# Optimization experiments

Hardware: AMD Instinct MI355X
Metric: run time of the kernel (lower is better)

The kernel has to match this reference:

```python
import jax, jax.numpy as jnp
import numpy as np

NSAMPLE = 32
EPS = 1e-5


def _fps(xyz, npoint):
    # xyz: [B, N, 3] -> indices [B, npoint] (farthest point sampling, start at idx 0)
    B, N, _ = xyz.shape
    def body(i, state):
        idx, dist, far = state
        idx = idx.at[:, i].set(far)
        centroid = jnp.take_along_axis(xyz, far[:, None, None], axis=1)  # [B,1,3]
        d = jnp.sum((xyz - centroid) ** 2, axis=-1)                      # [B,N]
        dist = jnp.minimum(dist, d)
        far = jnp.argmax(dist, axis=-1).astype(jnp.int32)
        return idx, dist, far
    idx0 = jnp.zeros((B, npoint), jnp.int32)
    dist0 = jnp.full((B, N), 1e10, xyz.dtype)
    far0 = jnp.zeros((B,), jnp.int32)
    idx, _, _ = jax.lax.fori_loop(0, npoint, body, (idx0, dist0, far0))
    return idx


def _knn(query, ref, k):
    # query [B,S,3], ref [B,N,3] -> neighbor idx [B,S,k]
    d = (jnp.sum(query * query, -1)[:, :, None]
         - 2.0 * jnp.einsum('bsc,bnc->bsn', query, ref)
         + jnp.sum(ref * ref, -1)[:, None, :])
    _, idx = jax.lax.top_k(-d, k)
    return idx


def _gather(x, idx):
    # x [B,N,C], idx [B,S,K] -> [B,S,K,C]
    B, S, K = idx.shape
    out = jnp.take_along_axis(x, idx.reshape(B, S * K)[..., None], axis=1)
    return out.reshape(B, S, K, x.shape[-1])


def _set_abstraction(xyz, feat, npoint, weights):
    # xyz [B,N,3], feat [B,N,C]
    fidx = _fps(xyz, npoint)
    new_xyz = jnp.take_along_axis(xyz, fidx[..., None], axis=1)        # [B,S,3]
    nidx = _knn(new_xyz, xyz, NSAMPLE)                                 # [B,S,K]
    g_xyz = _gather(xyz, nidx) - new_xyz[:, :, None, :]                # [B,S,K,3]
    g_feat = _gather(feat, nidx)                                       # [B,S,K,C]
    x = jnp.concatenate([g_xyz, g_feat], axis=-1)                      # [B,S,K,3+C]
    for W in weights:  # 1x1 conv == per-point matmul, then InstanceNorm2d (affine=False) + ReLU
        x = jnp.einsum('bskc,cd->bskd', x, W)
        mu = jnp.mean(x, axis=(1, 2), keepdims=True)
        var = jnp.var(x, axis=(1, 2), keepdims=True)
        x = jax.nn.relu((x - mu) * jax.lax.rsqrt(var + EPS))
    new_feat = jnp.max(x, axis=2)                                      # [B,S,Cout]
    return new_xyz, new_feat, fidx


def setup_inputs() -> dict:
    key = jax.random.key(0)
    ks = jax.random.split(key, 8)
    B, N = 4, 16384
    pc = jax.random.normal(ks[0], (B, 3, N), jnp.float32)
    feature = jax.random.normal(ks[1], (B, 3, N), jnp.float32)
    def w(k, cin, cout):
        return jax.random.normal(k, (cin, cout), jnp.float32) / np.sqrt(cin).astype(np.float32)
    return {
        'pc': pc, 'feature': feature,
        'sa1_w1': w(ks[2], 6, 32),  'sa1_w2': w(ks[3], 32, 32), 'sa1_w3': w(ks[4], 32, 32),
        'sa2_w1': w(ks[5], 35, 64), 'sa2_w2': w(ks[6], 64, 64), 'sa2_w3': w(ks[7], 64, 64),
    }


def reference(pc, feature, sa1_w1, sa1_w2, sa1_w3, sa2_w1, sa2_w2, sa2_w3):
    NPOINT = 4096
    xyz = jnp.transpose(pc, (0, 2, 1))       # [B,N,3]
    feat = jnp.transpose(feature, (0, 2, 1))  # [B,N,3]
    xyz1, feat1, fidx1 = _set_abstraction(xyz, feat, NPOINT // 2, [sa1_w1, sa1_w2, sa1_w3])
    xyz2, feat2, fidx2 = _set_abstraction(xyz1, feat1, NPOINT // 4, [sa2_w1, sa2_w2, sa2_w3])
    # match torch channel-first layout on outputs
    pc_l1 = jnp.transpose(xyz1, (0, 2, 1))
    pc_l2 = jnp.transpose(xyz2, (0, 2, 1))
    feat_l2 = jnp.transpose(feat2, (0, 2, 1))  # [B,64,NPOINT//4]
    return (pc, pc_l1, pc_l2, feat_l2, fidx1, fidx2)
```

## Files before the change

### kernel.cpp

```cpp
#include <hip/hip_runtime.h>
#include <math.h>

namespace {

constexpr int BB = 4;
constexpr int N0 = 16384;
constexpr int S1 = 2048;
constexpr int S2 = 1024;

__device__ __forceinline__ float sq3(float x, float y, float z){
  #pragma clang fp contract(off)
  return x*x + y*y + z*z;
}
__device__ __forceinline__ float sqdist(float ax,float ay,float az,float bx,float by,float bz){
  #pragma clang fp contract(off)
  float dx = ax-bx; float dy = ay-by; float dz = az-bz;
  return dx*dx + dy*dy + dz*dz;
}
__device__ __forceinline__ float dot3(float ax,float ay,float az,float bx,float by,float bz){
  #pragma clang fp contract(off)
  return ax*bx + ay*by + az*bz;
}
__device__ __forceinline__ float knndist(float qs, float dot, float rs){
  #pragma clang fp contract(off)
  return (qs - 2.0f*dot) + rs;
}

__global__ __launch_bounds__(256) void k_setup(const float* __restrict__ pc,
                                               const float* __restrict__ feat,
                                               float* __restrict__ out_pc,
                                               float* __restrict__ xyz,
                                               float* __restrict__ fN,
                                               float* __restrict__ rsq0)
{
  int t = blockIdx.x*256 + threadIdx.x;
  if (t < BB*3*N0) out_pc[t] = pc[t];
  if (t < BB*N0){
    int b = t >> 14, n = t & (N0-1);
    const float* p = pc + (size_t)b*3*N0;
    float x = p[n], y = p[N0+n], z = p[2*N0+n];
    float* q = xyz + (size_t)t*3;
    q[0]=x; q[1]=y; q[2]=z;
    rsq0[t] = sq3(x,y,z);
    const float* f = feat + (size_t)b*3*N0;
    float* g = fN + (size_t)t*3;
    g[0]=f[n]; g[1]=f[N0+n]; g[2]=f[2*N0+n];
  }
}

__device__ __forceinline__ void fps_writeout(int b, int i, float cx, float cy, float cz, int far,
                                             float* sxyz, float* srsq, float* pcl, float* fidxf, int NP)
{
  fidxf[(size_t)b*NP + i] = (float)far;
  float* o = sxyz + ((size_t)b*NP + i)*3;
  o[0]=cx; o[1]=cy; o[2]=cz;
  float* pb = pcl + (size_t)b*3*NP;
  pb[i] = cx; pb[NP+i] = cy; pb[2*NP+i] = cz;
  srsq[(size_t)b*NP + i] = sq3(cx,cy,cz);
}

template<int N, int NP, int BS, int PPT>
__global__ __launch_bounds__(BS) void k_fps(const float* __restrict__ pts,
                                            float* __restrict__ sxyz,
                                            float* __restrict__ srsq,
                                            float* __restrict__ pcl,
                                            float* __restrict__ fidxf)
{
  static_assert(N == BS*PPT, "bad fps shape");
  constexpr int NW = BS/64;
  int b = blockIdx.x, t = threadIdx.x;
  int lane = t & 63;
  int wid  = t >> 6;
  const float* P = pts + (size_t)b*N*3;
  float px[PPT], py[PPT], pz[PPT], dist[PPT];
  #pragma unroll
  for (int j=0;j<PPT;j++){
    int g = t + BS*j;
    px[j]=P[g*3]; py[j]=P[g*3+1]; pz[j]=P[g*3+2];
    dist[j]=1e10f;
  }
  __shared__ unsigned long long slot[2][NW];
  float cx = P[0], cy = P[1], cz = P[2];
  if (t == 0) fps_writeout(b, 0, cx, cy, cz, 0, sxyz, srsq, pcl, fidxf, NP);
  for (int i=1;i<NP;i++){
    int par = i & 1;
    float msq = -1.0f;
    #pragma unroll
    for (int j=0;j<PPT;j++){
      float d  = sqdist(px[j],py[j],pz[j],cx,cy,cz);
      float nd = fminf(dist[j], d);
      dist[j]  = nd;
      msq = fmaxf(msq, nd);
    }
    float s = sqrtf(msq);
    unsigned xb = __float_as_uint(msq);
    while (xb > 0u && sqrtf(__uint_as_float(xb - 1u)) == s) xb--;
    float lo = __uint_as_float(xb);
    int li = 0x7FFFFFFF;
    #pragma unroll
    for (int j=PPT-1;j>=0;j--) if (dist[j] >= lo) li = t + BS*j;
    unsigned long long key = ((unsigned long long)__float_as_uint(s) << 32)
                           | (unsigned long long)(unsigned)(~li);
    #pragma unroll
    for (int off=32; off>0; off>>=1){
      unsigned long long o = __shfl_xor(key, off);
      key = (o > key) ? o : key;
    }
    if (lane == 0) slot[par][wid] = key;
    __syncthreads();
    unsigned long long best = slot[par][0];
    #pragma unroll
    for (int w=1; w<NW; w++){
      unsigned long long o = slot[par][w];
      best = (o > best) ? o : best;
    }
    int far = (int)(~(unsigned)best);
    far = __builtin_amdgcn_readfirstlane(far);
    cx = P[(size_t)far*3]; cy = P[(size_t)far*3+1]; cz = P[(size_t)far*3+2];
    if (t == 0) fps_writeout(b, i, cx, cy, cz, far, sxyz, srsq, pcl, fidxf, NP);
  }
}

template<int NREF, int PPT, int NQ>
__global__ __launch_bounds__(512) void k_knn(const float* __restrict__ qxyz,
                                             const float* __restrict__ qrsq,
                                             const float* __restrict__ rxyz,
                                             const float* __restrict__ rrsq,
                                             int* __restrict__ nidx)
{
  static_assert(NREF == 512*PPT, "bad knn shape");
  int q = blockIdx.x;
  int b = q / NQ;
  int t = threadIdx.x;
  const float* R  = rxyz + (size_t)b*NREF*3;
  const float* RS = rrsq + (size_t)b*NREF;
  float qx = qxyz[(size_t)q*3], qy = qxyz[(size_t)q*3+1], qz = qxyz[(size_t)q*3+2];
  float qs = qrsq[q];
  unsigned u[PPT];
  #pragma unroll
  for (int j=0;j<PPT;j++){
    int g = t + 512*j;
    float rx=R[g*3], ry=R[g*3+1], rz=R[g*3+2];
    float d = knndist(qs, dot3(qx,qy,qz,rx,ry,rz), RS[g]);
    unsigned bu = __float_as_uint(d);
    u[j] = ((int)bu < 0) ? ~bu : (bu | 0x80000000u);
  }
  __shared__ unsigned hist[256];
  __shared__ unsigned s_pref, s_pm, s_want, s_cnteq;
  __shared__ int s_n;
  __shared__ int s_eq[1024];
  __shared__ int s_ne;
  if (t == 0){ s_pref=0u; s_pm=0u; s_want=32u; s_n=0; s_ne=0; }

  for (int shift=24; shift>=0; shift-=8){
    if (t < 256) hist[t] = 0u;
    __syncthreads();
    unsigned pref = s_pref, pm = s_pm;
    #pragma unroll
    for (int j=0;j<PPT;j++){
      if ((u[j] & pm) == pref) atomicAdd(&hist[(u[j]>>shift)&255], 1u);
    }
    __syncthreads();
    if (t < 64){
      unsigned h0=hist[4*t], h1=hist[4*t+1], h2=hist[4*t+2], h3=hist[4*t+3];
      unsigned ssum = h0+h1+h2+h3;
      unsigned inc = ssum;
      #pragma unroll
      for (int off=1; off<64; off<<=1){
        unsigned o = __shfl_up(inc, off);
        if (t >= off) inc += o;
      }
      unsigned exc = inc - ssum;
      unsigned want = s_want;
      if (exc < want && want <= inc){
        unsigned rem = want - exc;
        unsigned bin, below;
        if      (rem <= h0)       { bin=4*t+0; below=exc; }
        else if (rem <= h0+h1)    { bin=4*t+1; below=exc+h0; }
        else if (rem <= h0+h1+h2) { bin=4*t+2; below=exc+h0+h1; }
        else                      { bin=4*t+3; below=exc+h0+h1+h2; }
        s_pref = pref | (bin << shift);
        s_pm   = pm   | (0xFFu << shift);
        s_want = want - below;
        if (shift == 0) s_cnteq = hist[bin];
      }
    }
    __syncthreads();
  }
  unsigned T = s_pref;
  unsigned krem = s_want;
  unsigned cnteq = s_cnteq;
  int* outq = nidx + (size_t)q*32;
  #pragma unroll
  for (int j=0;j<PPT;j++){
    if (u[j] < T){ int p = atomicAdd(&s_n, 1); outq[p] = t + 512*j; }
  }
  __syncthreads();
  if (cnteq == krem){
    #pragma unroll
    for (int j=0;j<PPT;j++){
      if (u[j] == T){ int p = atomicAdd(&s_n, 1); outq[p] = t + 512*j; }
    }
  } else {
    #pragma unroll
    for (int j=0;j<PPT;j++){
      if (u[j] == T){ int p = atomicAdd(&s_ne, 1); if (p < 1024) s_eq[p] = t + 512*j; }
    }
    __syncthreads();
    if (t == 0){
      int ne = s_ne; if (ne > 1024) ne = 1024;
      int p = s_n;
      int take = (int)krem; if (take > ne) take = ne;
      for (int r=0; r<take; r++){
        int mn = 0x7FFFFFFF, mi = -1;
        for (int e=0; e<ne; e++){ if (s_eq[e] < mn){ mn = s_eq[e]; mi = e; } }
        if (mi < 0) break;
        outq[p++] = mn;
        s_eq[mi] = 0x7FFFFFFF;
      }
    }
  }
}

template<int C>
__device__ __forceinline__ void accum_sums(const float* o, int b, float* sums){
  __shared__ float s_sum[C];
  __shared__ float s_ssq[C];
  int t = threadIdx.x;
  if (t < C){ s_sum[t]=0.f; s_ssq[t]=0.f; }
  __syncthreads();
  int lane = t & 63;
  #pragma unroll
  for (int c=0;c<C;c++){
    float v = o[c], v2 = v*v;
    #pragma unroll
    for (int off=32; off>0; off>>=1){ v += __shfl_down(v, off); v2 += __shfl_down(v2, off); }
    if (lane == 0){ atomicAdd(&s_sum[c], v); atomicAdd(&s_ssq[c], v2); }
  }
  __syncthreads();
  if (t < C){
    atomicAdd(&sums[(b*64+t)*2],   s_sum[t]);
    atomicAdd(&sums[(b*64+t)*2+1], s_ssq[t]);
  }
}

__global__ __launch_bounds__(256) void k_sa1_l1(const float* __restrict__ xyz,
                                                const float* __restrict__ fN,
                                                const float* __restrict__ sxyz,
                                                const int* __restrict__ nidx,
                                                const float* __restrict__ W,
                                                float* __restrict__ xout,
                                                float* __restrict__ sums)
{
  __shared__ float sW[192];
  int t = threadIdx.x;
  if (t < 192) sW[t] = W[t];
  int row = blockIdx.x*256 + t;
  int b = row >> 16;
  int sk = row & 65535;
  int s = sk >> 5;
  int nb = nidx[row];
  const float* pr = xyz  + ((size_t)(b*N0 + nb))*3;
  const float* pq = sxyz + ((size_t)(b*S1 + s ))*3;
  const float* pf = fN   + ((size_t)(b*N0 + nb))*3;
  float i0 = pr[0]-pq[0], i1 = pr[1]-pq[1], i2 = pr[2]-pq[2];
  float i3 = pf[0], i4 = pf[1], i5 = pf[2];
  __syncthreads();
  float o[32];
  #pragma unroll
  for (int c=0;c<32;c++){
    float a = i0*sW[c];
    a = fmaf(i1, sW[ 32+c], a);
    a = fmaf(i2, sW[ 64+c], a);
    a = fmaf(i3, sW[ 96+c], a);
    a = fmaf(i4, sW[128+c], a);
    a = fmaf(i5, sW[160+c], a);
    o[c] = a;
    xout[(size_t)c*262144 + row] = a;
  }
  accum_sums<32>(o, b, sums);
}

template<int CIN, int COUT, int LRPB>
__global__ __launch_bounds__(256) void k_sa_mid(const float* __restrict__ xin,
                                                const float* __restrict__ W,
                                                const float* __restrict__ sums_in,
                                                float* __restrict__ xout,
                                                float* __restrict__ sums_out,
                                                int rows_total, float invM)
{
  __shared__ float sW[CIN*COUT];
  __shared__ float s_mu[CIN];
  __shared__ float s_rs[CIN];
  int t = threadIdx.x;
  int row = blockIdx.x*256 + t;
  int bb = (blockIdx.x*256) >> LRPB;
  for (int i=t; i<CIN*COUT; i+=256) sW[i] = W[i];
  if (t < CIN){
    float sm = sums_in[(bb*64+t)*2], sq = sums_in[(bb*64+t)*2+1];
    float mu = sm*invM;
    float var = fmaxf(sq*invM - mu*mu, 0.f);
    s_mu[t] = mu;
    s_rs[t] = 1.0f/sqrtf(var + 1e-5f);
  }
  __syncthreads();
  float o[COUT];
  #pragma unroll
  for (int d=0;d<COUT;d++) o[d] = 0.f;
  #pragma unroll
  for (int c=0;c<CIN;c++){
    float x = xin[(size_t)c*rows_total + row];
    float v = fmaxf((x - s_mu[c])*s_rs[c], 0.f);
    #pragma unroll
    for (int d=0;d<COUT;d++) o[d] = fmaf(v, sW[c*COUT+d], o[d]);
  }
  #pragma unroll
  for (int d=0;d<COUT;d++) xout[(size_t)d*rows_total + row] = o[d];
  accum_sums<COUT>(o, bb, sums_out);
}

__global__ __launch_bounds__(256) void k_sa2_l1(const float* __restrict__ xyz1,
                                                const float* __restrict__ feat1,
                                                const float* __restrict__ xyz2,
                                                const int* __restrict__ nidx,
                                                const float* __restrict__ W,
                                                float* __restrict__ xout,
                                                float* __restrict__ sums)
{
  __shared__ float sW[35*64];
  int t = threadIdx.x;
  for (int i=t; i<35*64; i+=256) sW[i] = W[i];
  int row = blockIdx.x*256 + t;
  int b = row >> 15;
  int sk = row & 32767;
  int s = sk >> 5;
  int nb = nidx[row];
  const float* pr = xyz1 + ((size_t)(b*S1 + nb))*3;
  const float* pq = xyz2 + ((size_t)(b*S2 + s ))*3;
  const float* pf = feat1 + ((size_t)(b*S1 + nb))*32;
  float i0 = pr[0]-pq[0], i1 = pr[1]-pq[1], i2 = pr[2]-pq[2];
  float fv[32];
  #pragma unroll
  for (int c=0;c<32;c++) fv[c] = pf[c];
  __syncthreads();
  float o[64];
  #pragma unroll
  for (int d=0;d<64;d++){
    float a = i0*sW[d];
    a = fmaf(i1, sW[ 64+d], a);
    a = fmaf(i2, sW[128+d], a);
    o[d] = a;
  }
  #pragma unroll
  for (int c=0;c<32;c++){
    float v = fv[c];
    #pragma unroll
    for (int d=0;d<64;d++) o[d] = fmaf(v, sW[(3+c)*64+d], o[d]);
  }
  #pragma unroll
  for (int d=0;d<64;d++) xout[(size_t)d*131072 + row] = o[d];
  accum_sums<64>(o, b, sums);
}

template<int C, int PTSB, int CF>
__global__ __launch_bounds__(256) void k_pool(const float* __restrict__ xin,
                                              const float* __restrict__ sums_in,
                                              float* __restrict__ out,
                                              int rows_total, float invM)
{
  int t = threadIdx.x;
  int c = t & (C-1);
  int pl = t / C;
  int p = blockIdx.x*(256/C) + pl;
  int b = p / PTSB;
  float sm = sums_in[(b*64+c)*2], sq = sums_in[(b*64+c)*2+1];
  float mu = sm*invM;
  float var = fmaxf(sq*invM - mu*mu, 0.f);
  float rs = 1.0f/sqrtf(var + 1e-5f);
  const float* xp = xin + (size_t)c*rows_total + (size_t)p*32;
  float m = -1e30f;
  #pragma unroll
  for (int k=0;k<32;k++) m = fmaxf(m, xp[k]);
  m = fmaxf((m - mu)*rs, 0.0f);
  if (CF) out[((size_t)(b*C + c))*PTSB + (p - b*PTSB)] = m;
  else    out[(size_t)p*C + c] = m;
}

constexpr size_t WS_XYZ   = 0;
constexpr size_t WS_FN    = WS_XYZ   + 196608;
constexpr size_t WS_RSQ0  = WS_FN    + 196608;
constexpr size_t WS_XYZ1  = WS_RSQ0  + 65536;
constexpr size_t WS_RSQ1  = WS_XYZ1  + 24576;
constexpr size_t WS_XYZ2  = WS_RSQ1  + 8192;
constexpr size_t WS_RSQ2  = WS_XYZ2  + 12288;
constexpr size_t WS_FEAT1 = WS_RSQ2  + 4096;
constexpr size_t WS_SUMS  = WS_FEAT1 + 262144;
constexpr size_t WS_BUFA  = WS_SUMS  + 3072;
constexpr size_t WS_BUFB  = WS_BUFA  + 8388608;
constexpr size_t WS_NIDX1 = WS_BUFB  + 8388608;
constexpr size_t WS_NIDX2 = WS_NIDX1 + 262144;

constexpr size_t OUT1 = 196608;
constexpr size_t OUT2 = 221184;
constexpr size_t OUT3 = 233472;
constexpr size_t OUT4 = 495616;
constexpr size_t OUT5 = 503808;

}

extern "C" void kernel_launch(void* const* d_in, const int* in_sizes, int n_in,
                              void* d_out, int out_size, void* d_ws, size_t ws_size,
                              hipStream_t stream)
{
  (void)in_sizes; (void)n_in; (void)out_size; (void)ws_size;
  const float* pc   = (const float*)d_in[0];
  const float* feat = (const float*)d_in[1];
  const float* W1 = (const float*)d_in[2];
  const float* W2 = (const float*)d_in[3];
  const float* W3 = (const float*)d_in[4];
  const float* W4 = (const float*)d_in[5];
  const float* W5 = (const float*)d_in[6];
  const float* W6 = (const float*)d_in[7];
  float* out = (float*)d_out;
  float* ws  = (float*)d_ws;

  float* xyz   = ws + WS_XYZ;
  float* fN    = ws + WS_FN;
  float* rsq0  = ws + WS_RSQ0;
  float* xyz1  = ws + WS_XYZ1;
  float* rsq1  = ws + WS_RSQ1;
  float* xyz2  = ws + WS_XYZ2;
  float* rsq2  = ws + WS_RSQ2;
  float* feat1 = ws + WS_FEAT1;
  float* sums  = ws + WS_SUMS;
  float* bufA  = ws + WS_BUFA;
  float* bufB  = ws + WS_BUFB;
  int* nidx1   = (int*)(ws + WS_NIDX1);
  int* nidx2   = (int*)(ws + WS_NIDX2);

  (void)hipMemsetAsync(sums, 0, 3072*sizeof(float), stream);

  k_setup<<<768, 256, 0, stream>>>(pc, feat, out, xyz, fN, rsq0);

  k_fps<N0, S1, 512, 32><<<BB, 512, 0, stream>>>(xyz, xyz1, rsq1, out+OUT1, out+OUT4);
  k_knn<N0, 32, S1><<<BB*S1, 512, 0, stream>>>(xyz1, rsq1, xyz, rsq0, nidx1);
  k_sa1_l1<<<1024, 256, 0, stream>>>(xyz, fN, xyz1, nidx1, W1, bufA, sums);
  k_sa_mid<32,32,16><<<1024, 256, 0, stream>>>(bufA, W2, sums,       bufB, sums+512,  262144, 1.0f/65536.0f);
  k_sa_mid<32,32,16><<<1024, 256, 0, stream>>>(bufB, W3, sums+512,   bufA, sums+1024, 262144, 1.0f/65536.0f);
  k_pool<32, 2048, 0><<<1024, 256, 0, stream>>>(bufA, sums+1024, feat1, 262144, 1.0f/65536.0f);

  k_fps<S1, S2, 512, 4><<<BB, 512, 0, stream>>>(xyz1, xyz2, rsq2, out+OUT2, out+OUT5);
  k_knn<S1, 4, S2><<<BB*S2, 512, 0, stream>>>(xyz2, rsq2, xyz1, rsq1, nidx2);
  k_sa2_l1<<<512, 256, 0, stream>>>(xyz1, feat1, xyz2, nidx2, W4, bufB, sums+1536);
  k_sa_mid<64,64,15><<<512, 256, 0, stream>>>(bufB, W5, sums+1536, bufA, sums+2048, 131072, 1.0f/32768.0f);
  k_sa_mid<64,64,15><<<512, 256, 0, stream>>>(bufA, W6, sums+2048, bufB, sums+2560, 131072, 1.0f/32768.0f);
  k_pool<64, 1024, 1><<<1024, 256, 0, stream>>>(bufB, sums+2560, out+OUT3, 131072, 1.0f/32768.0f);
}
```

Before: 7.162 ms.

## Restructure FPS: spill x/y to LDS, wider blocks, cheaper wave reduction

Result: slower. 8.457 ms (+18.1%).

```diff
diff --git a/kernel.cpp b/kernel.cpp
--- a/kernel.cpp
+++ b/kernel.cpp
@@ -59,39 +59,66 @@
   srsq[(size_t)b*NP + i] = sq3(cx,cy,cz);
 }
 
-template<int N, int NP, int BS, int PPT>
-__global__ __launch_bounds__(BS) void k_fps(const float* __restrict__ pts,
-                                            float* __restrict__ sxyz,
-                                            float* __restrict__ srsq,
-                                            float* __restrict__ pcl,
-                                            float* __restrict__ fidxf)
+template<int N, int NP, int BS, int PPT, int JL, int MINW>
+__global__ __launch_bounds__(BS, MINW) void k_fps(const float* __restrict__ pts,
+                                                  float* __restrict__ sxyz,
+                                                  float* __restrict__ srsq,
+                                                  float* __restrict__ pcl,
+                                                  float* __restrict__ fidxf)
 {
   static_assert(N == BS*PPT, "bad fps shape");
+  static_assert(JL <= PPT, "bad JL");
   constexpr int NW = BS/64;
+  constexpr int RR = PPT - JL;
   int b = blockIdx.x, t = threadIdx.x;
   int lane = t & 63;
   int wid  = t >> 6;
   const float* P = pts + (size_t)b*N*3;
-  float px[PPT], py[PPT], pz[PPT], dist[PPT];
-  #pragma unroll
-  for (int j=0;j<PPT;j++){
+
+  __shared__ float2 sxy[BS*JL];
+  __shared__ unsigned long long slot[2][NW];
+
+  float zr[PPT], dist[PPT];
+  float xr[RR ? RR : 1], yr[RR ? RR : 1];
+  #pragma unroll
+  for (int j=0;j<JL;j++){
     int g = t + BS*j;
-    px[j]=P[g*3]; py[j]=P[g*3+1]; pz[j]=P[g*3+2];
-    dist[j]=1e10f;
-  }
-  __shared__ unsigned long long slot[2][NW];
+    sxy[g] = make_float2(P[g*3], P[g*3+1]);
+    zr[j] = P[g*3+2];
+    dist[j] = 1e10f;
+  }
+  #pragma unroll
+  for (int r=0;r<RR;r++){
+    int j = JL + r;
+    int g = t + BS*j;
+    xr[r] = P[g*3]; yr[r] = P[g*3+1]; zr[j] = P[g*3+2];
+    dist[j] = 1e10f;
+  }
+
   float cx = P[0], cy = P[1], cz = P[2];
   if (t == 0) fps_writeout(b, 0, cx, cy, cz, 0, sxyz, srsq, pcl, fidxf, NP);
+
   for (int i=1;i<NP;i++){
     int par = i & 1;
     float msq = -1.0f;
     #pragma unroll
-    for (int j=0;j<PPT;j++){
-      float d  = sqdist(px[j],py[j],pz[j],cx,cy,cz);
+    for (int j=0;j<JL;j++){
+      float2 xy = sxy[t + BS*j];
+      float d  = sqdist(xy.x, xy.y, zr[j], cx, cy, cz);
       float nd = fminf(dist[j], d);
       dist[j]  = nd;
       msq = fmaxf(msq, nd);
     }
+    #pragma unroll
+    for (int r=0;r<RR;r++){
+      int j = JL + r;
+      float d  = sqdist(xr[r], yr[r], zr[j], cx, cy, cz);
+      float nd = fminf(dist[j], d);
+      dist[j]  = nd;
+      msq = fmaxf(msq, nd);
+    }
+    #pragma unroll
+    for (int off=32; off>0; off>>=1) msq = fmaxf(msq, __shfl_xor(msq, off));
     float s = sqrtf(msq);
     unsigned xb = __float_as_uint(msq);
     while (xb > 0u && sqrtf(__uint_as_float(xb - 1u)) == s) xb--;
@@ -99,14 +126,11 @@
     int li = 0x7FFFFFFF;
     #pragma unroll
     for (int j=PPT-1;j>=0;j--) if (dist[j] >= lo) li = t + BS*j;
-    unsigned long long key = ((unsigned long long)__float_as_uint(s) << 32)
-                           | (unsigned long long)(unsigned)(~li);
-    #pragma unroll
-    for (int off=32; off>0; off>>=1){
-      unsigned long long o = __shfl_xor(key, off);
-      key = (o > key) ? o : key;
-    }
-    if (lane == 0) slot[par][wid] = key;
+    #pragma unroll
+    for (int off=32; off>0; off>>=1) li = min(li, __shfl_xor(li, off));
+    if (lane == 0)
+      slot[par][wid] = ((unsigned long long)__float_as_uint(s) << 32)
+                     | (unsigned long long)(unsigned)(~li);
     __syncthreads();
     unsigned long long best = slot[par][0];
     #pragma unroll
@@ -442,14 +466,14 @@
 
   k_setup<<<768, 256, 0, stream>>>(pc, feat, out, xyz, fN, rsq0);
 
-  k_fps<N0, S1, 512, 32><<<BB, 512, 0, stream>>>(xyz, xyz1, rsq1, out+OUT1, out+OUT4);
+  k_fps<N0, S1, 1024, 16, 15, 4><<<BB, 1024, 0, stream>>>(xyz, xyz1, rsq1, out+OUT1, out+OUT4);
   k_knn<N0, 32, S1><<<BB*S1, 512, 0, stream>>>(xyz1, rsq1, xyz, rsq0, nidx1);
   k_sa1_l1<<<1024, 256, 0, stream>>>(xyz, fN, xyz1, nidx1, W1, bufA, sums);
   k_sa_mid<32,32,16><<<1024, 256, 0, stream>>>(bufA, W2, sums,       bufB, sums+512,  262144, 1.0f/65536.0f);
   k_sa_mid<32,32,16><<<1024, 256, 0, stream>>>(bufB, W3, sums+512,   bufA, sums+1024, 262144, 1.0f/65536.0f);
   k_pool<32, 2048, 0><<<1024, 256, 0, stream>>>(bufA, sums+1024, feat1, 262144, 1.0f/65536.0f);
 
-  k_fps<S1, S2, 512, 4><<<BB, 512, 0, stream>>>(xyz1, xyz2, rsq2, out+OUT2, out+OUT5);
+  k_fps<S1, S2, 256, 8, 8, 1><<<BB, 256, 0, stream>>>(xyz1, xyz2, rsq2, out+OUT2, out+OUT5);
   k_knn<S1, 4, S2><<<BB*S2, 512, 0, stream>>>(xyz2, rsq2, xyz1, rsq1, nidx2);
   k_sa2_l1<<<512, 256, 0, stream>>>(xyz1, feat1, xyz2, nidx2, W4, bufB, sums+1536);
   k_sa_mid<64,64,15><<<512, 256, 0, stream>>>(bufB, W5, sums+1536, bufA, sums+2048, 131072, 1.0f/32768.0f);
```
